# Kernel optimization log

Measured on AMD Instinct MI355X. Metric: run time of the kernel, lower is better.

Reference implementation:

```python
import jax, jax.numpy as jnp
import numpy as np

# Dimensions / config (WorldModelConfig + PredictiveLayerConfig defaults)
S, N, L = 128, 256, 3          # n_sensory, n_hidden, n_layers
T, B = 100, 512                # timesteps, batch
TAU_MEM, TAU_PRED, DT = 20.0, 50.0, 1.0
NOISE_STD, ERROR_GAIN = 0.02, 0.5
DECAY_MEM = float(np.exp(-DT / TAU_MEM))
DECAY_PRED = float(np.exp(-DT / TAU_PRED))
ALPHA = DT / TAU_PRED          # precision EMA rate


def setup_inputs() -> dict:
    key = jax.random.key(0)
    ks = jax.random.split(key, 12)
    w = lambda k, a, b, s: jax.random.normal(k, (a, b), dtype=jnp.float32) * s
    return {
        'sensory_seq': jax.random.uniform(ks[0], (T, B, S), dtype=jnp.float32),
        'ff0': w(ks[1], S, N, 0.1 / S ** 0.5),
        'ff1': w(ks[2], N, N, 0.1 / N ** 0.5),
        'ff2': w(ks[3], N, N, 0.1 / N ** 0.5),
        'rec0': w(ks[4], N, N, 0.01),
        'rec1': w(ks[5], N, N, 0.01),
        'rec2': w(ks[6], N, N, 0.01),
        'pred0': w(ks[7], N, N, 0.1 / N ** 0.5),
        'pred1': w(ks[8], N, N, 0.1 / N ** 0.5),
        'p2r0': w(ks[9], N, N, 0.1 / N ** 0.5),
        'p2r1': w(ks[10], N, N, 0.1 / N ** 0.5),
    }


def _lif(v, inp, decay, noise):
    """LIF membrane update: leak + drive + noise, threshold=1.0, reset to 0."""
    v = decay * v + inp + noise
    s = (v >= 1.0).astype(v.dtype)
    return s, v * (1.0 - s)


def reference(sensory_seq, ff0, ff1, ff2, rec0, rec1, rec2, pred0, pred1, p2r0, p2r1):
    ffs = [ff0, ff1, ff2]
    recs = [rec0, rec1, rec2]
    preds = [pred0, pred1]
    p2rs = [p2r0, p2r1]
    mask = 1.0 - jnp.eye(N, dtype=sensory_seq.dtype)   # recurrent_mask
    base_key = jax.random.key(42)
    Bsz = sensory_seq.shape[1]

    init = (
        jnp.zeros((L, Bsz, N), jnp.float32),   # repr membrane
        jnp.zeros((2, Bsz, N), jnp.float32),   # pred membrane (layers 0,1)
        jnp.zeros((L, Bsz, N), jnp.float32),   # last spikes
        jnp.ones((L, Bsz, N), jnp.float32),    # precision
    )

    def step(carry, t):
        v, pv, last, prec = carry
        nks = jax.random.split(jax.random.fold_in(base_key, t), 5)
        new_v, new_pv, new_last, new_prec, errs = [], [], [], [], []
        for i in range(L):
            # top-down prediction from layer i+1's previous-step activity
            if i < L - 1:
                pred_in = last[i + 1] @ preds[i]
                pn = (NOISE_STD * 0.5) * jax.random.normal(nks[3 + i], (Bsz, N))
                psp, pvi = _lif(pv[i], pred_in, DECAY_PRED, pn)
                prediction = psp @ p2rs[i]
                new_pv.append(pvi)
            else:
                prediction = jnp.zeros((Bsz, N), jnp.float32)
            # bottom-up input: sensory for layer 0, lower layer's current spikes above
            inp_act = sensory_seq[t] if i == 0 else new_last[i - 1]
            input_repr = inp_act @ ffs[i]
            error = input_repr - prediction
            total = prediction + error * ERROR_GAIN * prec[i] + last[i] @ (recs[i] * mask)
            noi = NOISE_STD * jax.random.normal(nks[i], (Bsz, N))
            sp, vi = _lif(v[i], total, DECAY_MEM, noi)
            # precision EMA on inverse error variance
            ev = jnp.mean(error * error, axis=1, keepdims=True) + 1e-6
            pr = (1.0 - ALPHA) * prec[i] + ALPHA * (1.0 / ev)
            new_v.append(vi); new_last.append(sp); new_prec.append(pr); errs.append(error)
        carry = (jnp.stack(new_v), jnp.stack(new_pv), jnp.stack(new_last), jnp.stack(new_prec))
        return carry, jnp.stack(errs)   # [L, B, N] per step

    _, errors = jax.lax.scan(step, init, jnp.arange(T))
    return errors   # [T, L, B, N]
```

## Files before the change

kernel.cpp:

```cpp
#include <hip/hip_runtime.h>
#include <stdint.h>

#define TSTEPS 100
#define BATCH  512
#define NH     256
#define NS     128

__device__ __forceinline__ uint32_t rotl32(uint32_t x, int r) {
  return (x << r) | (x >> (32 - r));
}

__device__ __forceinline__ void tf2x32(uint32_t k0, uint32_t k1,
                                       uint32_t c0, uint32_t c1,
                                       uint32_t& o0, uint32_t& o1) {
  const uint32_t ks2 = k0 ^ k1 ^ 0x1BD11BDAu;
  uint32_t x0 = c0 + k0, x1 = c1 + k1;
#define TFR(r) { x0 += x1; x1 = rotl32(x1, r); x1 ^= x0; }
  TFR(13) TFR(15) TFR(26) TFR(6)
  x0 += k1;  x1 += ks2 + 1u;
  TFR(17) TFR(29) TFR(16) TFR(24)
  x0 += ks2; x1 += k0 + 2u;
  TFR(13) TFR(15) TFR(26) TFR(6)
  x0 += k0;  x1 += k1 + 3u;
  TFR(17) TFR(29) TFR(16) TFR(24)
  x0 += k1;  x1 += ks2 + 4u;
  TFR(13) TFR(15) TFR(26) TFR(6)
  x0 += ks2; x1 += k0 + 5u;
#undef TFR
  o0 = x0; o1 = x1;
}

__device__ __forceinline__ float xla_vf32_log(float a) {
  uint32_t bits = __float_as_uint(a);
  float e = __fadd_rn((float)((int)(bits >> 23) - 127), 1.0f);
  float x = __uint_as_float((bits & 0x007FFFFFu) | 0x3F000000u);
  const bool mask = x < 0.707106781186547524f;
  float tmp = mask ? x : 0.0f;
  x = __fsub_rn(x, 1.0f);
  e = mask ? __fsub_rn(e, 1.0f) : e;
  x = __fadd_rn(x, tmp);
  float z = __fmul_rn(x, x);
  float y = 7.0376836292e-2f;
  y = __fmaf_rn(y, x, -1.1514610310e-1f);
  y = __fmaf_rn(y, x, 1.1676998740e-1f);
  y = __fmaf_rn(y, x, -1.2420140846e-1f);
  y = __fmaf_rn(y, x, 1.4249322787e-1f);
  y = __fmaf_rn(y, x, -1.6668057665e-1f);
  y = __fmaf_rn(y, x, 2.0000714765e-1f);
  y = __fmaf_rn(y, x, -2.4999993993e-1f);
  y = __fmaf_rn(y, x, 3.3333331174e-1f);
  y = __fmul_rn(y, x);
  y = __fmul_rn(y, z);
  y = __fmaf_rn(e, -2.12194440e-4f, y);
  y = __fmaf_rn(-0.5f, z, y);
  x = __fadd_rn(x, y);
  x = __fmaf_rn(e, 0.693359375f, x);
  return x;
}

__device__ __forceinline__ float xla_sqrt2_erfinv(float u) {
  float nxx = -__fmul_rn(u, u);
  float w;
  if (fabsf(nxx) < 1e-4f) {
    w = -__fmul_rn(__fmaf_rn(-0.5f, nxx, 1.0f), nxx);
  } else {
    w = -xla_vf32_log(__fadd_rn(nxx, 1.0f));
  }
  float p;
  if (w < 5.0f) {
    float t = __fsub_rn(w, 2.5f);
    p = 2.81022636e-08f;
    p = __fmaf_rn(p, t, 3.43273939e-07f);
    p = __fmaf_rn(p, t, -3.5233877e-06f);
    p = __fmaf_rn(p, t, -4.39150654e-06f);
    p = __fmaf_rn(p, t, 0.00021858087f);
    p = __fmaf_rn(p, t, -0.00125372503f);
    p = __fmaf_rn(p, t, -0.00417768164f);
    p = __fmaf_rn(p, t, 0.246640727f);
    p = __fmaf_rn(p, t, 1.50140941f);
  } else {
    float t = __fsub_rn(__fsqrt_rn(w), 3.0f);
    p = -0.000200214257f;
    p = __fmaf_rn(p, t, 0.000100950558f);
    p = __fmaf_rn(p, t, 0.00134934322f);
    p = __fmaf_rn(p, t, -0.00367342844f);
    p = __fmaf_rn(p, t, 0.00573950773f);
    p = __fmaf_rn(p, t, -0.0076224613f);
    p = __fmaf_rn(p, t, 0.00943887047f);
    p = __fmaf_rn(p, t, 1.00167406f);
    p = __fmaf_rn(p, t, 2.83297682f);
  }
  return __fmul_rn((float)1.4142135623730951, __fmul_rn(p, u));
}

__device__ __forceinline__ float jax_normal(uint32_t k0, uint32_t k1, uint32_t j) {
  uint32_t o0, o1;
  tf2x32(k0, k1, 0u, j, o0, o1);
  const uint32_t bits = o0 ^ o1;
  float f = __fsub_rn(__uint_as_float((bits >> 9) | 0x3f800000u), 1.0f);
  const float LO = -0.99999994f;
  float u = __fmaf_rn(f, 2.0f, LO);
  u = fmaxf(LO, u);
  return xla_sqrt2_erfinv(u);
}


__device__ __forceinline__ void dot1_seg(const float4* __restrict__ P0,
                                         const float* __restrict__ A0,
                                         int n, int k4b, int k4e, float& r0) {
  float a0 = r0;
  #pragma unroll 8
  for (int k4 = k4b; k4 < k4e; ++k4) {
    float4 w0 = P0[k4 * NH + n];
    float4 x0 = *reinterpret_cast<const float4*>(A0 + 4 * k4);
    a0 = __fmaf_rn(x0.x, w0.x, a0); a0 = __fmaf_rn(x0.y, w0.y, a0);
    a0 = __fmaf_rn(x0.z, w0.z, a0); a0 = __fmaf_rn(x0.w, w0.w, a0);
  }
  r0 = a0;
}

__device__ __forceinline__ void dot2_seg(const float4* __restrict__ P0,
                                         const float* __restrict__ A0,
                                         const float4* __restrict__ P1,
                                         const float* __restrict__ A1,
                                         int n, int k4b, int k4e,
                                         float& r0, float& r1) {
  float a0 = r0, a1 = r1;
  #pragma unroll 8
  for (int k4 = k4b; k4 < k4e; ++k4) {
    float4 w0 = P0[k4 * NH + n];
    float4 w1 = P1[k4 * NH + n];
    float4 x0 = *reinterpret_cast<const float4*>(A0 + 4 * k4);
    float4 x1 = *reinterpret_cast<const float4*>(A1 + 4 * k4);
    a0 = __fmaf_rn(x0.x, w0.x, a0); a0 = __fmaf_rn(x0.y, w0.y, a0);
    a0 = __fmaf_rn(x0.z, w0.z, a0); a0 = __fmaf_rn(x0.w, w0.w, a0);
    a1 = __fmaf_rn(x1.x, w1.x, a1); a1 = __fmaf_rn(x1.y, w1.y, a1);
    a1 = __fmaf_rn(x1.z, w1.z, a1); a1 = __fmaf_rn(x1.w, w1.w, a1);
  }
  r0 = a0; r1 = a1;
}

__device__ __forceinline__ void dot3_seg(const float4* __restrict__ P0,
                                         const float* __restrict__ A0,
                                         const float4* __restrict__ P1,
                                         const float* __restrict__ A1,
                                         const float4* __restrict__ P2,
                                         const float* __restrict__ A2,
                                         int n, int k4b, int k4e,
                                         float& r0, float& r1, float& r2) {
  float a0 = r0, a1 = r1, a2 = r2;
  #pragma unroll 4
  for (int k4 = k4b; k4 < k4e; ++k4) {
    float4 w0 = P0[k4 * NH + n];
    float4 w1 = P1[k4 * NH + n];
    float4 w2 = P2[k4 * NH + n];
    float4 x0 = *reinterpret_cast<const float4*>(A0 + 4 * k4);
    float4 x1 = *reinterpret_cast<const float4*>(A1 + 4 * k4);
    float4 x2 = *reinterpret_cast<const float4*>(A2 + 4 * k4);
    a0 = __fmaf_rn(x0.x, w0.x, a0); a0 = __fmaf_rn(x0.y, w0.y, a0);
    a0 = __fmaf_rn(x0.z, w0.z, a0); a0 = __fmaf_rn(x0.w, w0.w, a0);
    a1 = __fmaf_rn(x1.x, w1.x, a1); a1 = __fmaf_rn(x1.y, w1.y, a1);
    a1 = __fmaf_rn(x1.z, w1.z, a1); a1 = __fmaf_rn(x1.w, w1.w, a1);
    a2 = __fmaf_rn(x2.x, w2.x, a2); a2 = __fmaf_rn(x2.y, w2.y, a2);
    a2 = __fmaf_rn(x2.z, w2.z, a2); a2 = __fmaf_rn(x2.w, w2.w, a2);
  }
  r0 = a0; r1 = a1; r2 = a2;
}

__global__ void pack_w(const float* __restrict__ src, float* __restrict__ dst,
                       int K, int zero_diag) {
  int tid = blockIdx.x * 256 + threadIdx.x;
  if (tid >= K * NH) return;
  int k = tid >> 8, n = tid & 255;
  float v = src[tid];
  if (zero_diag && k == n) v = 0.f;
  dst[(((k >> 2) * NH) + n) * 4 + (k & 3)] = v;
}

__global__ __launch_bounds__(256)
void gen_noise(float* __restrict__ NZ) {
  uint32_t idx = blockIdx.x * 256u + threadIdx.x;
  uint32_t j = idx & 131071u;
  uint32_t td = idx >> 17;
  uint32_t t = td / 5u, d = td - 5u * t;
  uint32_t fk0, fk1, k0, k1;
  tf2x32(0u, 42u, 0u, t, fk0, fk1);
  tf2x32(fk0, fk1, 0u, d, k0, k1);
  float z = jax_normal(k0, k1, j);
  float scale = (d >= 3u) ? 0.01f : 0.02f;
  NZ[idx] = __fmul_rn(scale, z);
}

__global__ __launch_bounds__(NH)
void wm_kernel_fast(const float* __restrict__ sensory,
                    const float4* __restrict__ pred0p, const float4* __restrict__ pred1p,
                    const float4* __restrict__ p2r0p,  const float4* __restrict__ rec0p,
                    const float4* __restrict__ ff0p,   const float4* __restrict__ p2r1p,
                    const float4* __restrict__ ff1p,   const float4* __restrict__ rec1p,
                    const float4* __restrict__ ff2p,   const float4* __restrict__ rec2p,
                    const float* __restrict__ NZ,
                    float* __restrict__ out) {
  const int b = blockIdx.x;
  const int n = threadIdx.x;

  __shared__ __align__(16) float last[2][3][NH];
  __shared__ __align__(16) float psp0[NH];
  __shared__ __align__(16) float psp1[NH];
  __shared__ __align__(16) float sens[NS];
  __shared__ __align__(16) float errsq[3][NH];
  __shared__ float evsum[3];

  for (int i = 0; i < 3; ++i) { last[0][i][n] = 0.f; last[1][i][n] = 0.f; }

  float v0 = 0.f, v1 = 0.f, v2 = 0.f, pv0 = 0.f, pv1 = 0.f;
  float prec0 = 1.f, prec1 = 1.f, prec2 = 1.f;
  const float DM = (float)0.951229424500714009;
  const float DP = (float)0.980198673306755250;

  __syncthreads();

  for (int t = 0; t < TSTEPS; ++t) {
    const int p = t & 1, q = p ^ 1;
    const size_t nb = ((size_t)t * 5 * BATCH + b) * NH + n;

    if (n < NS) sens[n] = sensory[((size_t)t * BATCH + b) * NS + n];
    {
      float pn0 = NZ[nb + (size_t)3 * BATCH * NH];
      float pn1 = NZ[nb + (size_t)4 * BATCH * NH];
      float acc0 = 0.f, acc1 = 0.f;
      dot2_seg(pred0p, last[p][1], pred1p, last[p][2], n, 0, 64, acc0, acc1);
      pv0 = __fadd_rn(__fmaf_rn(DP, pv0, acc0), pn0);
      bool s0 = (pv0 >= 1.0f);
      psp0[n] = s0 ? 1.f : 0.f;
      pv0 = s0 ? 0.f : pv0;
      pv1 = __fadd_rn(__fmaf_rn(DP, pv1, acc1), pn1);
      bool s1 = (pv1 >= 1.0f);
      psp1[n] = s1 ? 1.f : 0.f;
      pv1 = s1 ? 0.f : pv1;
    }
    __syncthreads();

    {
      float noi = NZ[nb];
      float pr = 0.f, rc = 0.f, inp = 0.f;
      dot3_seg(p2r0p, psp0, rec0p, last[p][0], ff0p, sens, n, 0, 32, pr, rc, inp);
      dot2_seg(p2r0p, psp0, rec0p, last[p][0], n, 32, 64, pr, rc);
      float err = __fsub_rn(inp, pr);
      out[(((size_t)t * 3 + 0) * BATCH + b) * NH + n] = err;
      errsq[0][n] = __fmul_rn(err, err);
      float m1  = __fmul_rn(err, 0.5f);
      float tot = __fadd_rn(__fmaf_rn(m1, prec0, pr), rc);
      v0 = __fadd_rn(__fmaf_rn(DM, v0, tot), noi);
      bool s = (v0 >= 1.0f);
      last[q][0][n] = s ? 1.f : 0.f;
      v0 = s ? 0.f : v0;
    }
    __syncthreads();

    {
      float noi = NZ[nb + (size_t)1 * BATCH * NH];
      float pr = 0.f, inp = 0.f, rc = 0.f;
      dot3_seg(p2r1p, psp1, ff1p, last[q][0], rec1p, last[p][1], n, 0, 64,
               pr, inp, rc);
      float err = __fsub_rn(inp, pr);
      out[(((size_t)t * 3 + 1) * BATCH + b) * NH + n] = err;
      errsq[1][n] = __fmul_rn(err, err);
      float m1  = __fmul_rn(err, 0.5f);
      float tot = __fadd_rn(__fmaf_rn(m1, prec1, pr), rc);
      v1 = __fadd_rn(__fmaf_rn(DM, v1, tot), noi);
      bool s = (v1 >= 1.0f);
      last[q][1][n] = s ? 1.f : 0.f;
      v1 = s ? 0.f : v1;
    }
    __syncthreads();

    {
      float noi = NZ[nb + (size_t)2 * BATCH * NH];
      float inp = 0.f, rc = 0.f;
      dot2_seg(ff2p, last[q][1], rec2p, last[p][2], n, 0, 64, inp, rc);
      float err = inp;
      out[(((size_t)t * 3 + 2) * BATCH + b) * NH + n] = err;
      errsq[2][n] = __fmul_rn(err, err);
      float m1  = __fmul_rn(err, 0.5f);
      float tot = __fadd_rn(__fmaf_rn(m1, prec2, 0.0f), rc);
      v2 = __fadd_rn(__fmaf_rn(DM, v2, tot), noi);
      bool s = (v2 >= 1.0f);
      last[q][2][n] = s ? 1.f : 0.f;
      v2 = s ? 0.f : v2;
    }
    __syncthreads();

    if (((n & 63) == 0) && n < 192) {
      const float4* s4 = reinterpret_cast<const float4*>(errsq[n >> 6]);
      float acc = 0.f;
      #pragma unroll 16
      for (int k4 = 0; k4 < 64; ++k4) {
        float4 v = s4[k4];
        acc = __fadd_rn(acc, v.x); acc = __fadd_rn(acc, v.y);
        acc = __fadd_rn(acc, v.z); acc = __fadd_rn(acc, v.w);
      }
      evsum[n >> 6] = acc;
    }
    __syncthreads();

    {
      float ev0 = __fadd_rn(__fmul_rn(evsum[0], 0.00390625f), 1e-6f);
      float ev1 = __fadd_rn(__fmul_rn(evsum[1], 0.00390625f), 1e-6f);
      float ev2 = __fadd_rn(__fmul_rn(evsum[2], 0.00390625f), 1e-6f);
      prec0 = __fmaf_rn(0.98f, prec0, __fmul_rn(0.02f, 1.0f / ev0));
      prec1 = __fmaf_rn(0.98f, prec1, __fmul_rn(0.02f, 1.0f / ev1));
      prec2 = __fmaf_rn(0.98f, prec2, __fmul_rn(0.02f, 1.0f / ev2));
    }
  }
}

__device__ __forceinline__ float dot_lds(const float* __restrict__ a,
                                         const float* __restrict__ W,
                                         int n, int K) {
  float acc = 0.f;
  #pragma unroll 8
  for (int k = 0; k < K; ++k)
    acc = __fmaf_rn(a[k], W[k * NH + n], acc);
  return acc;
}

__device__ __forceinline__ float dot_rec(const float* __restrict__ a,
                                         const float* __restrict__ W, int n) {
  float acc = 0.f;
  #pragma unroll 8
  for (int k = 0; k < NH; ++k) {
    float w = (k == n) ? 0.f : W[k * NH + n];
    acc = __fmaf_rn(a[k], w, acc);
  }
  return acc;
}

__global__ __launch_bounds__(NH)
void wm_kernel_mono(const float* __restrict__ sensory,
                    const float* __restrict__ ff0, const float* __restrict__ ff1,
                    const float* __restrict__ ff2,
                    const float* __restrict__ rec0, const float* __restrict__ rec1,
                    const float* __restrict__ rec2,
                    const float* __restrict__ pred0, const float* __restrict__ pred1,
                    const float* __restrict__ p2r0, const float* __restrict__ p2r1,
                    float* __restrict__ out) {
  const int b = blockIdx.x;
  const int n = threadIdx.x;

  __shared__ float last[2][3][NH];
  __shared__ float psp[NH];
  __shared__ float sens[NS];
  __shared__ float errsq[3][NH];
  __shared__ float evsum[3];
  __shared__ uint32_t keys[TSTEPS][5][2];

  if (n < TSTEPS) {
    uint32_t fk0, fk1;
    tf2x32(0u, 42u, 0u, (uint32_t)n, fk0, fk1);
    #pragma unroll
    for (int i = 0; i < 5; ++i) {
      uint32_t s0, s1;
      tf2x32(fk0, fk1, 0u, (uint32_t)i, s0, s1);
      keys[n][i][0] = s0; keys[n][i][1] = s1;
    }
  }
  for (int i = 0; i < 3; ++i) { last[0][i][n] = 0.f; last[1][i][n] = 0.f; }

  float v0 = 0.f, v1 = 0.f, v2 = 0.f, pv0 = 0.f, pv1 = 0.f;
  float prec0 = 1.f, prec1 = 1.f, prec2 = 1.f;
  const float DM = (float)0.951229424500714009;
  const float DP = (float)0.980198673306755250;
  const uint32_t j = (uint32_t)(b * NH + n);

  __syncthreads();

  for (int t = 0; t < TSTEPS; ++t) {
    const int p = t & 1, q = p ^ 1;

    if (n < NS) sens[n] = sensory[((size_t)t * BATCH + b) * NS + n];
    {
      float acc = dot_lds(last[p][1], pred0, n, NH);
      float pn = __fmul_rn(0.01f, jax_normal(keys[t][3][0], keys[t][3][1], j));
      pv0 = __fadd_rn(__fmaf_rn(DP, pv0, acc), pn);
      bool s = (pv0 >= 1.0f);
      psp[n] = s ? 1.f : 0.f;
      pv0 = s ? 0.f : pv0;
    }
    __syncthreads();

    {
      float pr  = dot_lds(psp, p2r0, n, NH);
      float inp = dot_lds(sens, ff0, n, NS);
      float rc  = dot_rec(last[p][0], rec0, n);
      float err = __fsub_rn(inp, pr);
      out[(((size_t)t * 3 + 0) * BATCH + b) * NH + n] = err;
      errsq[0][n] = __fmul_rn(err, err);
      float m1  = __fmul_rn(err, 0.5f);
      float tot = __fadd_rn(__fmaf_rn(m1, prec0, pr), rc);
      float noi = __fmul_rn(0.02f, jax_normal(keys[t][0][0], keys[t][0][1], j));
      v0 = __fadd_rn(__fmaf_rn(DM, v0, tot), noi);
      bool s = (v0 >= 1.0f);
      last[q][0][n] = s ? 1.f : 0.f;
      v0 = s ? 0.f : v0;
    }
    __syncthreads();

    {
      float acc = dot_lds(last[p][2], pred1, n, NH);
      float pn = __fmul_rn(0.01f, jax_normal(keys[t][4][0], keys[t][4][1], j));
      pv1 = __fadd_rn(__fmaf_rn(DP, pv1, acc), pn);
      bool s = (pv1 >= 1.0f);
      psp[n] = s ? 1.f : 0.f;
      pv1 = s ? 0.f : pv1;
    }
    __syncthreads();

    {
      float pr  = dot_lds(psp, p2r1, n, NH);
      float inp = dot_lds(last[q][0], ff1, n, NH);
      float rc  = dot_rec(last[p][1], rec1, n);
      float err = __fsub_rn(inp, pr);
      out[(((size_t)t * 3 + 1) * BATCH + b) * NH + n] = err;
      errsq[1][n] = __fmul_rn(err, err);
      float m1  = __fmul_rn(err, 0.5f);
      float tot = __fadd_rn(__fmaf_rn(m1, prec1, pr), rc);
      float noi = __fmul_rn(0.02f, jax_normal(keys[t][1][0], keys[t][1][1], j));
      v1 = __fadd_rn(__fmaf_rn(DM, v1, tot), noi);
      bool s = (v1 >= 1.0f);
      last[q][1][n] = s ? 1.f : 0.f;
      v1 = s ? 0.f : v1;
    }
    __syncthreads();

    {
      float inp = dot_lds(last[q][1], ff2, n, NH);
      float rc  = dot_rec(last[p][2], rec2, n);
      float err = inp;
      out[(((size_t)t * 3 + 2) * BATCH + b) * NH + n] = err;
      errsq[2][n] = __fmul_rn(err, err);
      float m1  = __fmul_rn(err, 0.5f);
      float tot = __fadd_rn(__fmaf_rn(m1, prec2, 0.0f), rc);
      float noi = __fmul_rn(0.02f, jax_normal(keys[t][2][0], keys[t][2][1], j));
      v2 = __fadd_rn(__fmaf_rn(DM, v2, tot), noi);
      bool s = (v2 >= 1.0f);
      last[q][2][n] = s ? 1.f : 0.f;
      v2 = s ? 0.f : v2;
    }
    __syncthreads();

    if (((n & 63) == 0) && n < 192) {
      const float* s = errsq[n >> 6];
      float acc = 0.f;
      #pragma unroll 32
      for (int k = 0; k < NH; ++k) acc = __fadd_rn(acc, s[k]);
      evsum[n >> 6] = acc;
    }
    __syncthreads();

    {
      float ev0 = __fadd_rn(__fmul_rn(evsum[0], 0.00390625f), 1e-6f);
      float ev1 = __fadd_rn(__fmul_rn(evsum[1], 0.00390625f), 1e-6f);
      float ev2 = __fadd_rn(__fmul_rn(evsum[2], 0.00390625f), 1e-6f);
      prec0 = __fmaf_rn(0.98f, prec0, __fmul_rn(0.02f, 1.0f / ev0));
      prec1 = __fmaf_rn(0.98f, prec1, __fmul_rn(0.02f, 1.0f / ev1));
      prec2 = __fmaf_rn(0.98f, prec2, __fmul_rn(0.02f, 1.0f / ev2));
    }
  }
}

extern "C" void kernel_launch(void* const* d_in, const int* in_sizes, int n_in,
                              void* d_out, int out_size, void* d_ws, size_t ws_size,
                              hipStream_t stream) {
  (void)in_sizes; (void)n_in; (void)out_size;
  const float* sensory = (const float*)d_in[0];
  const float* ff0  = (const float*)d_in[1];
  const float* ff1  = (const float*)d_in[2];
  const float* ff2  = (const float*)d_in[3];
  const float* rec0 = (const float*)d_in[4];
  const float* rec1 = (const float*)d_in[5];
  const float* rec2 = (const float*)d_in[6];
  const float* pred0 = (const float*)d_in[7];
  const float* pred1 = (const float*)d_in[8];
  const float* p2r0 = (const float*)d_in[9];
  const float* p2r1 = (const float*)d_in[10];
  float* out = (float*)d_out;

  const size_t OFF_PRED0 = 0, OFF_PRED1 = 65536, OFF_P2R0 = 131072,
               OFF_REC0 = 196608, OFF_FF0 = 262144, OFF_P2R1 = 294912,
               OFF_FF1 = 360448, OFF_REC1 = 425984, OFF_FF2 = 491520,
               OFF_REC2 = 557056, OFF_NZ = 655360;
  const size_t NZ_FLOATS = (size_t)TSTEPS * 5 * BATCH * NH;
  const size_t NEED = (OFF_NZ + NZ_FLOATS) * sizeof(float);

  if (ws_size >= NEED) {
    float* W = (float*)d_ws;
    pack_w<<<dim3(NH * NH / 256), dim3(256), 0, stream>>>(pred0, W + OFF_PRED0, NH, 0);
    pack_w<<<dim3(NH * NH / 256), dim3(256), 0, stream>>>(pred1, W + OFF_PRED1, NH, 0);
    pack_w<<<dim3(NH * NH / 256), dim3(256), 0, stream>>>(p2r0,  W + OFF_P2R0,  NH, 0);
    pack_w<<<dim3(NH * NH / 256), dim3(256), 0, stream>>>(rec0,  W + OFF_REC0,  NH, 1);
    pack_w<<<dim3(NS * NH / 256), dim3(256), 0, stream>>>(ff0,   W + OFF_FF0,   NS, 0);
    pack_w<<<dim3(NH * NH / 256), dim3(256), 0, stream>>>(p2r1,  W + OFF_P2R1,  NH, 0);
    pack_w<<<dim3(NH * NH / 256), dim3(256), 0, stream>>>(ff1,   W + OFF_FF1,   NH, 0);
    pack_w<<<dim3(NH * NH / 256), dim3(256), 0, stream>>>(rec1,  W + OFF_REC1,  NH, 1);
    pack_w<<<dim3(NH * NH / 256), dim3(256), 0, stream>>>(ff2,   W + OFF_FF2,   NH, 0);
    pack_w<<<dim3(NH * NH / 256), dim3(256), 0, stream>>>(rec2,  W + OFF_REC2,  NH, 1);
    gen_noise<<<dim3((unsigned)(NZ_FLOATS / 256)), dim3(256), 0, stream>>>(W + OFF_NZ);
    wm_kernel_fast<<<dim3(BATCH), dim3(NH), 0, stream>>>(
        sensory,
        (const float4*)(W + OFF_PRED0), (const float4*)(W + OFF_PRED1),
        (const float4*)(W + OFF_P2R0),  (const float4*)(W + OFF_REC0),
        (const float4*)(W + OFF_FF0),   (const float4*)(W + OFF_P2R1),
        (const float4*)(W + OFF_FF1),   (const float4*)(W + OFF_REC1),
        (const float4*)(W + OFF_FF2),   (const float4*)(W + OFF_REC2),
        W + OFF_NZ, out);
  } else {
    wm_kernel_mono<<<dim3(BATCH), dim3(NH), 0, stream>>>(
        sensory, ff0, ff1, ff2, rec0, rec1, rec2,
        pred0, pred1, p2r0, p2r1, out);
  }
}
```

Before: 4.600 ms.

## Process two batch rows per block so paired lanes share weight loads

Replaces the one-batch-per-block kernel with a 512-thread block handling two batch rows, interleaving lanes so neighbouring threads compute the same hidden unit for different rows. Weight float4 loads are shared across the lane pair, aiming to halve weight fetch traffic per output. In exchange, output and noise accesses become interleaved across rows (less contiguous), and block-level syncs now cover twice the threads.

```diff
diff --git a/kernel.cpp b/kernel.cpp
--- a/kernel.cpp
+++ b/kernel.cpp
@@ -104,6 +104,29 @@
   return xla_sqrt2_erfinv(u);
 }
 
+__global__ void pack_w(const float* __restrict__ src, float* __restrict__ dst,
+                       int K, int zero_diag) {
+  int tid = blockIdx.x * 256 + threadIdx.x;
+  if (tid >= K * NH) return;
+  int k = tid >> 8, n = tid & 255;
+  float v = src[tid];
+  if (zero_diag && k == n) v = 0.f;
+  dst[(((k >> 2) * NH) + n) * 4 + (k & 3)] = v;
+}
+
+__global__ __launch_bounds__(256)
+void gen_noise(float* __restrict__ NZ) {
+  uint32_t idx = blockIdx.x * 256u + threadIdx.x;
+  uint32_t j = idx & 131071u;
+  uint32_t td = idx >> 17;
+  uint32_t t = td / 5u, d = td - 5u * t;
+  uint32_t fk0, fk1, k0, k1;
+  tf2x32(0u, 42u, 0u, t, fk0, fk1);
+  tf2x32(fk0, fk1, 0u, d, k0, k1);
+  float z = jax_normal(k0, k1, j);
+  float scale = (d >= 3u) ? 0.01f : 0.02f;
+  NZ[idx] = __fmul_rn(scale, z);
+}
 
 __device__ __forceinline__ void dot1_seg(const float4* __restrict__ P0,
                                          const float* __restrict__ A0,
@@ -167,50 +190,32 @@
   r0 = a0; r1 = a1; r2 = a2;
 }
 
-__global__ void pack_w(const float* __restrict__ src, float* __restrict__ dst,
-                       int K, int zero_diag) {
-  int tid = blockIdx.x * 256 + threadIdx.x;
-  if (tid >= K * NH) return;
-  int k = tid >> 8, n = tid & 255;
-  float v = src[tid];
-  if (zero_diag && k == n) v = 0.f;
-  dst[(((k >> 2) * NH) + n) * 4 + (k & 3)] = v;
-}
-
-__global__ __launch_bounds__(256)
-void gen_noise(float* __restrict__ NZ) {
-  uint32_t idx = blockIdx.x * 256u + threadIdx.x;
-  uint32_t j = idx & 131071u;
-  uint32_t td = idx >> 17;
-  uint32_t t = td / 5u, d = td - 5u * t;
-  uint32_t fk0, fk1, k0, k1;
-  tf2x32(0u, 42u, 0u, t, fk0, fk1);
-  tf2x32(fk0, fk1, 0u, d, k0, k1);
-  float z = jax_normal(k0, k1, j);
-  float scale = (d >= 3u) ? 0.01f : 0.02f;
-  NZ[idx] = __fmul_rn(scale, z);
-}
-
-__global__ __launch_bounds__(NH)
-void wm_kernel_fast(const float* __restrict__ sensory,
-                    const float4* __restrict__ pred0p, const float4* __restrict__ pred1p,
-                    const float4* __restrict__ p2r0p,  const float4* __restrict__ rec0p,
-                    const float4* __restrict__ ff0p,   const float4* __restrict__ p2r1p,
-                    const float4* __restrict__ ff1p,   const float4* __restrict__ rec1p,
-                    const float4* __restrict__ ff2p,   const float4* __restrict__ rec2p,
-                    const float* __restrict__ NZ,
-                    float* __restrict__ out) {
-  const int b = blockIdx.x;
-  const int n = threadIdx.x;
-
-  __shared__ __align__(16) float last[2][3][NH];
-  __shared__ __align__(16) float psp0[NH];
-  __shared__ __align__(16) float psp1[NH];
-  __shared__ __align__(16) float sens[NS];
-  __shared__ __align__(16) float errsq[3][NH];
-  __shared__ float evsum[3];
-
-  for (int i = 0; i < 3; ++i) { last[0][i][n] = 0.f; last[1][i][n] = 0.f; }
+__global__ __launch_bounds__(512)
+void wm_fast4(const float* __restrict__ sensory,
+              const float4* __restrict__ pred0p, const float4* __restrict__ pred1p,
+              const float4* __restrict__ p2r0p,  const float4* __restrict__ rec0p,
+              const float4* __restrict__ ff0p,   const float4* __restrict__ p2r1p,
+              const float4* __restrict__ ff1p,   const float4* __restrict__ rec1p,
+              const float4* __restrict__ ff2p,   const float4* __restrict__ rec2p,
+              const float* __restrict__ NZ,
+              float* __restrict__ out) {
+  const int tid = threadIdx.x;
+  const int n = tid >> 1;
+  const int r = tid & 1;
+  const int b = blockIdx.x * 2 + r;
+
+  __shared__ __align__(16) float last[2][3][2][NH];
+  __shared__ __align__(16) float psp0[2][NH];
+  __shared__ __align__(16) float psp1[2][NH];
+  __shared__ __align__(16) float sens[2][NS];
+  __shared__ __align__(16) float errsq[3][2][NH];
+  __shared__ float evsum[3][2];
+
+  #pragma unroll
+  for (int i = 0; i < 3; ++i) {
+    last[0][i][r][n] = 0.f;
+    last[1][i][r][n] = 0.f;
+  }
 
   float v0 = 0.f, v1 = 0.f, v2 = 0.f, pv0 = 0.f, pv1 = 0.f;
   float prec0 = 1.f, prec1 = 1.f, prec2 = 1.f;
@@ -223,19 +228,22 @@
     const int p = t & 1, q = p ^ 1;
     const size_t nb = ((size_t)t * 5 * BATCH + b) * NH + n;
 
-    if (n < NS) sens[n] = sensory[((size_t)t * BATCH + b) * NS + n];
+    if (tid < 2 * NS) {
+      int rr = tid >> 7, kk = tid & 127;
+      sens[rr][kk] = sensory[((size_t)t * BATCH + blockIdx.x * 2 + rr) * NS + kk];
+    }
     {
       float pn0 = NZ[nb + (size_t)3 * BATCH * NH];
       float pn1 = NZ[nb + (size_t)4 * BATCH * NH];
       float acc0 = 0.f, acc1 = 0.f;
-      dot2_seg(pred0p, last[p][1], pred1p, last[p][2], n, 0, 64, acc0, acc1);
+      dot2_seg(pred0p, last[p][1][r], pred1p, last[p][2][r], n, 0, 64, acc0, acc1);
       pv0 = __fadd_rn(__fmaf_rn(DP, pv0, acc0), pn0);
       bool s0 = (pv0 >= 1.0f);
-      psp0[n] = s0 ? 1.f : 0.f;
+      psp0[r][n] = s0 ? 1.f : 0.f;
       pv0 = s0 ? 0.f : pv0;
       pv1 = __fadd_rn(__fmaf_rn(DP, pv1, acc1), pn1);
       bool s1 = (pv1 >= 1.0f);
-      psp1[n] = s1 ? 1.f : 0.f;
+      psp1[r][n] = s1 ? 1.f : 0.f;
       pv1 = s1 ? 0.f : pv1;
     }
     __syncthreads();
@@ -243,16 +251,17 @@
     {
       float noi = NZ[nb];
       float pr = 0.f, rc = 0.f, inp = 0.f;
-      dot3_seg(p2r0p, psp0, rec0p, last[p][0], ff0p, sens, n, 0, 32, pr, rc, inp);
-      dot2_seg(p2r0p, psp0, rec0p, last[p][0], n, 32, 64, pr, rc);
+      dot3_seg(p2r0p, psp0[r], rec0p, last[p][0][r], ff0p, sens[r], n, 0, 32,
+               pr, rc, inp);
+      dot2_seg(p2r0p, psp0[r], rec0p, last[p][0][r], n, 32, 64, pr, rc);
       float err = __fsub_rn(inp, pr);
       out[(((size_t)t * 3 + 0) * BATCH + b) * NH + n] = err;
-      errsq[0][n] = __fmul_rn(err, err);
+      errsq[0][r][n] = __fmul_rn(err, err);
       float m1  = __fmul_rn(err, 0.5f);
       float tot = __fadd_rn(__fmaf_rn(m1, prec0, pr), rc);
       v0 = __fadd_rn(__fmaf_rn(DM, v0, tot), noi);
       bool s = (v0 >= 1.0f);
-      last[q][0][n] = s ? 1.f : 0.f;
+      last[q][0][r][n] = s ? 1.f : 0.f;
       v0 = s ? 0.f : v0;
     }
     __syncthreads();
@@ -260,16 +269,16 @@
     {
       float noi = NZ[nb + (size_t)1 * BATCH * NH];
       float pr = 0.f, inp = 0.f, rc = 0.f;
-      dot3_seg(p2r1p, psp1, ff1p, last[q][0], rec1p, last[p][1], n, 0, 64,
-               pr, inp, rc);
+      dot3_seg(p2r1p, psp1[r], ff1p, last[q][0][r], rec1p, last[p][1][r],
+               n, 0, 64, pr, inp, rc);
       float err = __fsub_rn(inp, pr);
       out[(((size_t)t * 3 + 1) * BATCH + b) * NH + n] = err;
-      errsq[1][n] = __fmul_rn(err, err);
+      errsq[1][r][n] = __fmul_rn(err, err);
       float m1  = __fmul_rn(err, 0.5f);
       float tot = __fadd_rn(__fmaf_rn(m1, prec1, pr), rc);
       v1 = __fadd_rn(__fmaf_rn(DM, v1, tot), noi);
       bool s = (v1 >= 1.0f);
-      last[q][1][n] = s ? 1.f : 0.f;
+      last[q][1][r][n] = s ? 1.f : 0.f;
       v1 = s ? 0.f : v1;
     }
     __syncthreads();
@@ -277,21 +286,22 @@
     {
       float noi = NZ[nb + (size_t)2 * BATCH * NH];
       float inp = 0.f, rc = 0.f;
-      dot2_seg(ff2p, last[q][1], rec2p, last[p][2], n, 0, 64, inp, rc);
+      dot2_seg(ff2p, last[q][1][r], rec2p, last[p][2][r], n, 0, 64, inp, rc);
       float err = inp;
       out[(((size_t)t * 3 + 2) * BATCH + b) * NH + n] = err;
-      errsq[2][n] = __fmul_rn(err, err);
+      errsq[2][r][n] = __fmul_rn(err, err);
       float m1  = __fmul_rn(err, 0.5f);
       float tot = __fadd_rn(__fmaf_rn(m1, prec2, 0.0f), rc);
       v2 = __fadd_rn(__fmaf_rn(DM, v2, tot), noi);
       bool s = (v2 >= 1.0f);
-      last[q][2][n] = s ? 1.f : 0.f;
+      last[q][2][r][n] = s ? 1.f : 0.f;
       v2 = s ? 0.f : v2;
     }
     __syncthreads();
 
-    if (((n & 63) == 0) && n < 192) {
-      const float4* s4 = reinterpret_cast<const float4*>(errsq[n >> 6]);
+    if (tid < 6) {
+      const int l = tid >> 1, rr = tid & 1;
+      const float4* s4 = reinterpret_cast<const float4*>(errsq[l][rr]);
       float acc = 0.f;
       #pragma unroll 16
       for (int k4 = 0; k4 < 64; ++k4) {
@@ -299,14 +309,14 @@
         acc = __fadd_rn(acc, v.x); acc = __fadd_rn(acc, v.y);
         acc = __fadd_rn(acc, v.z); acc = __fadd_rn(acc, v.w);
       }
-      evsum[n >> 6] = acc;
-    }
-    __syncthreads();
-
-    {
-      float ev0 = __fadd_rn(__fmul_rn(evsum[0], 0.00390625f), 1e-6f);
-      float ev1 = __fadd_rn(__fmul_rn(evsum[1], 0.00390625f), 1e-6f);
-      float ev2 = __fadd_rn(__fmul_rn(evsum[2], 0.00390625f), 1e-6f);
+      evsum[l][rr] = acc;
+    }
+    __syncthreads();
+
+    {
+      float ev0 = __fadd_rn(__fmul_rn(evsum[0][r], 0.00390625f), 1e-6f);
+      float ev1 = __fadd_rn(__fmul_rn(evsum[1][r], 0.00390625f), 1e-6f);
+      float ev2 = __fadd_rn(__fmul_rn(evsum[2][r], 0.00390625f), 1e-6f);
       prec0 = __fmaf_rn(0.98f, prec0, __fmul_rn(0.02f, 1.0f / ev0));
       prec1 = __fmaf_rn(0.98f, prec1, __fmul_rn(0.02f, 1.0f / ev1));
       prec2 = __fmaf_rn(0.98f, prec2, __fmul_rn(0.02f, 1.0f / ev2));
@@ -505,7 +515,7 @@
     pack_w<<<dim3(NH * NH / 256), dim3(256), 0, stream>>>(ff2,   W + OFF_FF2,   NH, 0);
     pack_w<<<dim3(NH * NH / 256), dim3(256), 0, stream>>>(rec2,  W + OFF_REC2,  NH, 1);
     gen_noise<<<dim3((unsigned)(NZ_FLOATS / 256)), dim3(256), 0, stream>>>(W + OFF_NZ);
-    wm_kernel_fast<<<dim3(BATCH), dim3(NH), 0, stream>>>(
+    wm_fast4<<<dim3(BATCH / 2), dim3(512), 0, stream>>>(
         sensory,
         (const float4*)(W + OFF_PRED0), (const float4*)(W + OFF_PRED1),
         (const float4*)(W + OFF_P2R0),  (const float4*)(W + OFF_REC0),
```

Result: no change. 4.554 ms (-1.0%).

## Split each batch row's matvecs across two 256-thread halves per block

Applied to the files above, without the earlier changes.

Doubles the block size to 512 threads, so two half-blocks each handle one output neuron and share the per-step matrix-vector products. Partial results are exchanged through a shared-memory transfer buffer. This shortens the serial dot-product chain each thread runs per timestep and raises the number of waves per CU. The cost is extra barriers per step, idle halves during the elementwise updates, and more register and occupancy pressure with 512-thread blocks.

```diff
diff --git a/kernel.cpp b/kernel.cpp
--- a/kernel.cpp
+++ b/kernel.cpp
@@ -104,6 +104,29 @@
   return xla_sqrt2_erfinv(u);
 }
 
+__global__ void pack_w(const float* __restrict__ src, float* __restrict__ dst,
+                       int K, int zero_diag) {
+  int tid = blockIdx.x * 256 + threadIdx.x;
+  if (tid >= K * NH) return;
+  int k = tid >> 8, n = tid & 255;
+  float v = src[tid];
+  if (zero_diag && k == n) v = 0.f;
+  dst[(((k >> 2) * NH) + n) * 4 + (k & 3)] = v;
+}
+
+__global__ __launch_bounds__(256)
+void gen_noise(float* __restrict__ NZ) {
+  uint32_t idx = blockIdx.x * 256u + threadIdx.x;
+  uint32_t j = idx & 131071u;
+  uint32_t td = idx >> 17;
+  uint32_t t = td / 5u, d = td - 5u * t;
+  uint32_t fk0, fk1, k0, k1;
+  tf2x32(0u, 42u, 0u, t, fk0, fk1);
+  tf2x32(fk0, fk1, 0u, d, k0, k1);
+  float z = jax_normal(k0, k1, j);
+  float scale = (d >= 3u) ? 0.01f : 0.02f;
+  NZ[idx] = __fmul_rn(scale, z);
+}
 
 __device__ __forceinline__ void dot1_seg(const float4* __restrict__ P0,
                                          const float* __restrict__ A0,
@@ -140,79 +163,34 @@
   r0 = a0; r1 = a1;
 }
 
-__device__ __forceinline__ void dot3_seg(const float4* __restrict__ P0,
-                                         const float* __restrict__ A0,
-                                         const float4* __restrict__ P1,
-                                         const float* __restrict__ A1,
-                                         const float4* __restrict__ P2,
-                                         const float* __restrict__ A2,
-                                         int n, int k4b, int k4e,
-                                         float& r0, float& r1, float& r2) {
-  float a0 = r0, a1 = r1, a2 = r2;
-  #pragma unroll 4
-  for (int k4 = k4b; k4 < k4e; ++k4) {
-    float4 w0 = P0[k4 * NH + n];
-    float4 w1 = P1[k4 * NH + n];
-    float4 w2 = P2[k4 * NH + n];
-    float4 x0 = *reinterpret_cast<const float4*>(A0 + 4 * k4);
-    float4 x1 = *reinterpret_cast<const float4*>(A1 + 4 * k4);
-    float4 x2 = *reinterpret_cast<const float4*>(A2 + 4 * k4);
-    a0 = __fmaf_rn(x0.x, w0.x, a0); a0 = __fmaf_rn(x0.y, w0.y, a0);
-    a0 = __fmaf_rn(x0.z, w0.z, a0); a0 = __fmaf_rn(x0.w, w0.w, a0);
-    a1 = __fmaf_rn(x1.x, w1.x, a1); a1 = __fmaf_rn(x1.y, w1.y, a1);
-    a1 = __fmaf_rn(x1.z, w1.z, a1); a1 = __fmaf_rn(x1.w, w1.w, a1);
-    a2 = __fmaf_rn(x2.x, w2.x, a2); a2 = __fmaf_rn(x2.y, w2.y, a2);
-    a2 = __fmaf_rn(x2.z, w2.z, a2); a2 = __fmaf_rn(x2.w, w2.w, a2);
-  }
-  r0 = a0; r1 = a1; r2 = a2;
-}
-
-__global__ void pack_w(const float* __restrict__ src, float* __restrict__ dst,
-                       int K, int zero_diag) {
-  int tid = blockIdx.x * 256 + threadIdx.x;
-  if (tid >= K * NH) return;
-  int k = tid >> 8, n = tid & 255;
-  float v = src[tid];
-  if (zero_diag && k == n) v = 0.f;
-  dst[(((k >> 2) * NH) + n) * 4 + (k & 3)] = v;
-}
-
-__global__ __launch_bounds__(256)
-void gen_noise(float* __restrict__ NZ) {
-  uint32_t idx = blockIdx.x * 256u + threadIdx.x;
-  uint32_t j = idx & 131071u;
-  uint32_t td = idx >> 17;
-  uint32_t t = td / 5u, d = td - 5u * t;
-  uint32_t fk0, fk1, k0, k1;
-  tf2x32(0u, 42u, 0u, t, fk0, fk1);
-  tf2x32(fk0, fk1, 0u, d, k0, k1);
-  float z = jax_normal(k0, k1, j);
-  float scale = (d >= 3u) ? 0.01f : 0.02f;
-  NZ[idx] = __fmul_rn(scale, z);
-}
-
-__global__ __launch_bounds__(NH)
-void wm_kernel_fast(const float* __restrict__ sensory,
-                    const float4* __restrict__ pred0p, const float4* __restrict__ pred1p,
-                    const float4* __restrict__ p2r0p,  const float4* __restrict__ rec0p,
-                    const float4* __restrict__ ff0p,   const float4* __restrict__ p2r1p,
-                    const float4* __restrict__ ff1p,   const float4* __restrict__ rec1p,
-                    const float4* __restrict__ ff2p,   const float4* __restrict__ rec2p,
-                    const float* __restrict__ NZ,
-                    float* __restrict__ out) {
+__global__ __launch_bounds__(512)
+void wm_fast5(const float* __restrict__ sensory,
+              const float4* __restrict__ pred0p, const float4* __restrict__ pred1p,
+              const float4* __restrict__ p2r0p,  const float4* __restrict__ rec0p,
+              const float4* __restrict__ ff0p,   const float4* __restrict__ p2r1p,
+              const float4* __restrict__ ff1p,   const float4* __restrict__ rec1p,
+              const float4* __restrict__ ff2p,   const float4* __restrict__ rec2p,
+              const float* __restrict__ NZ,
+              float* __restrict__ out) {
+  const int tid = threadIdx.x;
+  const int n = tid & 255;
+  const int h = tid >> 8;
   const int b = blockIdx.x;
-  const int n = threadIdx.x;
 
   __shared__ __align__(16) float last[2][3][NH];
   __shared__ __align__(16) float psp0[NH];
   __shared__ __align__(16) float psp1[NH];
   __shared__ __align__(16) float sens[NS];
   __shared__ __align__(16) float errsq[3][NH];
+  __shared__ __align__(16) float xfer[NH];
   __shared__ float evsum[3];
 
-  for (int i = 0; i < 3; ++i) { last[0][i][n] = 0.f; last[1][i][n] = 0.f; }
-
-  float v0 = 0.f, v1 = 0.f, v2 = 0.f, pv0 = 0.f, pv1 = 0.f;
+  if (h == 0) {
+    #pragma unroll
+    for (int i = 0; i < 3; ++i) { last[0][i][n] = 0.f; last[1][i][n] = 0.f; }
+  }
+
+  float pv = 0.f, vA = 0.f, vB = 0.f;
   float prec0 = 1.f, prec1 = 1.f, prec2 = 1.f;
   const float DM = (float)0.951229424500714009;
   const float DP = (float)0.980198673306755250;
@@ -223,75 +201,104 @@
     const int p = t & 1, q = p ^ 1;
     const size_t nb = ((size_t)t * 5 * BATCH + b) * NH + n;
 
-    if (n < NS) sens[n] = sensory[((size_t)t * BATCH + b) * NS + n];
-    {
-      float pn0 = NZ[nb + (size_t)3 * BATCH * NH];
-      float pn1 = NZ[nb + (size_t)4 * BATCH * NH];
-      float acc0 = 0.f, acc1 = 0.f;
-      dot2_seg(pred0p, last[p][1], pred1p, last[p][2], n, 0, 64, acc0, acc1);
-      pv0 = __fadd_rn(__fmaf_rn(DP, pv0, acc0), pn0);
-      bool s0 = (pv0 >= 1.0f);
-      psp0[n] = s0 ? 1.f : 0.f;
-      pv0 = s0 ? 0.f : pv0;
-      pv1 = __fadd_rn(__fmaf_rn(DP, pv1, acc1), pn1);
-      bool s1 = (pv1 >= 1.0f);
-      psp1[n] = s1 ? 1.f : 0.f;
-      pv1 = s1 ? 0.f : pv1;
-    }
-    __syncthreads();
-
-    {
+    if (tid < NS) sens[tid] = sensory[((size_t)t * BATCH + b) * NS + tid];
+    if (h == 0) {
+      float acc = 0.f;
+      dot1_seg(pred0p, last[p][1], n, 0, 64, acc);
+      float pn = NZ[nb + (size_t)3 * BATCH * NH];
+      pv = __fadd_rn(__fmaf_rn(DP, pv, acc), pn);
+      bool s = (pv >= 1.0f);
+      psp0[n] = s ? 1.f : 0.f;
+      pv = s ? 0.f : pv;
+    } else {
+      float acc = 0.f;
+      dot1_seg(pred1p, last[p][2], n, 0, 64, acc);
+      float pn = NZ[nb + (size_t)4 * BATCH * NH];
+      pv = __fadd_rn(__fmaf_rn(DP, pv, acc), pn);
+      bool s = (pv >= 1.0f);
+      psp1[n] = s ? 1.f : 0.f;
+      pv = s ? 0.f : pv;
+    }
+    __syncthreads();
+
+    float inp_b = 0.f, rc_b = 0.f;
+    if (h == 0) {
+      dot2_seg(ff0p, sens, rec0p, last[p][0], n, 0, 32, inp_b, rc_b);
+      dot1_seg(rec0p, last[p][0], n, 32, 64, rc_b);
+    } else {
+      float pr = 0.f;
+      dot1_seg(p2r0p, psp0, n, 0, 64, pr);
+      xfer[n] = pr;
+    }
+    __syncthreads();
+    if (h == 0) {
+      float pr = xfer[n];
       float noi = NZ[nb];
-      float pr = 0.f, rc = 0.f, inp = 0.f;
-      dot3_seg(p2r0p, psp0, rec0p, last[p][0], ff0p, sens, n, 0, 32, pr, rc, inp);
-      dot2_seg(p2r0p, psp0, rec0p, last[p][0], n, 32, 64, pr, rc);
-      float err = __fsub_rn(inp, pr);
+      float err = __fsub_rn(inp_b, pr);
       out[(((size_t)t * 3 + 0) * BATCH + b) * NH + n] = err;
       errsq[0][n] = __fmul_rn(err, err);
       float m1  = __fmul_rn(err, 0.5f);
-      float tot = __fadd_rn(__fmaf_rn(m1, prec0, pr), rc);
-      v0 = __fadd_rn(__fmaf_rn(DM, v0, tot), noi);
-      bool s = (v0 >= 1.0f);
+      float tot = __fadd_rn(__fmaf_rn(m1, prec0, pr), rc_b);
+      vA = __fadd_rn(__fmaf_rn(DM, vA, tot), noi);
+      bool s = (vA >= 1.0f);
       last[q][0][n] = s ? 1.f : 0.f;
-      v0 = s ? 0.f : v0;
-    }
-    __syncthreads();
-
-    {
+      vA = s ? 0.f : vA;
+    }
+    __syncthreads();
+
+    if (h == 0) {
+      float inp = 0.f;
+      dot1_seg(ff1p, last[q][0], n, 0, 64, inp);
+      xfer[n] = inp;
+    } else {
+      float pr = 0.f, rc = 0.f;
+      dot2_seg(p2r1p, psp1, rec1p, last[p][1], n, 0, 64, pr, rc);
+      inp_b = pr; rc_b = rc;
+    }
+    __syncthreads();
+    if (h == 1) {
+      float pr = inp_b, rc = rc_b;
+      float inp = xfer[n];
       float noi = NZ[nb + (size_t)1 * BATCH * NH];
-      float pr = 0.f, inp = 0.f, rc = 0.f;
-      dot3_seg(p2r1p, psp1, ff1p, last[q][0], rec1p, last[p][1], n, 0, 64,
-               pr, inp, rc);
       float err = __fsub_rn(inp, pr);
       out[(((size_t)t * 3 + 1) * BATCH + b) * NH + n] = err;
       errsq[1][n] = __fmul_rn(err, err);
       float m1  = __fmul_rn(err, 0.5f);
       float tot = __fadd_rn(__fmaf_rn(m1, prec1, pr), rc);
-      v1 = __fadd_rn(__fmaf_rn(DM, v1, tot), noi);
-      bool s = (v1 >= 1.0f);
+      vA = __fadd_rn(__fmaf_rn(DM, vA, tot), noi);
+      bool s = (vA >= 1.0f);
       last[q][1][n] = s ? 1.f : 0.f;
-      v1 = s ? 0.f : v1;
-    }
-    __syncthreads();
-
-    {
+      vA = s ? 0.f : vA;
+    }
+    __syncthreads();
+
+    if (h == 0) {
+      float inp = 0.f;
+      dot1_seg(ff2p, last[q][1], n, 0, 64, inp);
+      inp_b = inp;
+    } else {
+      float rc = 0.f;
+      dot1_seg(rec2p, last[p][2], n, 0, 64, rc);
+      xfer[n] = rc;
+    }
+    __syncthreads();
+    if (h == 0) {
+      float rc = xfer[n];
+      float err = inp_b;
       float noi = NZ[nb + (size_t)2 * BATCH * NH];
-      float inp = 0.f, rc = 0.f;
-      dot2_seg(ff2p, last[q][1], rec2p, last[p][2], n, 0, 64, inp, rc);
-      float err = inp;
       out[(((size_t)t * 3 + 2) * BATCH + b) * NH + n] = err;
       errsq[2][n] = __fmul_rn(err, err);
       float m1  = __fmul_rn(err, 0.5f);
       float tot = __fadd_rn(__fmaf_rn(m1, prec2, 0.0f), rc);
-      v2 = __fadd_rn(__fmaf_rn(DM, v2, tot), noi);
-      bool s = (v2 >= 1.0f);
+      vB = __fadd_rn(__fmaf_rn(DM, vB, tot), noi);
+      bool s = (vB >= 1.0f);
       last[q][2][n] = s ? 1.f : 0.f;
-      v2 = s ? 0.f : v2;
-    }
-    __syncthreads();
-
-    if (((n & 63) == 0) && n < 192) {
-      const float4* s4 = reinterpret_cast<const float4*>(errsq[n >> 6]);
+      vB = s ? 0.f : vB;
+    }
+    __syncthreads();
+
+    if (((tid & 63) == 0) && tid < 192) {
+      const float4* s4 = reinterpret_cast<const float4*>(errsq[tid >> 6]);
       float acc = 0.f;
       #pragma unroll 16
       for (int k4 = 0; k4 < 64; ++k4) {
@@ -299,7 +306,7 @@
         acc = __fadd_rn(acc, v.x); acc = __fadd_rn(acc, v.y);
         acc = __fadd_rn(acc, v.z); acc = __fadd_rn(acc, v.w);
       }
-      evsum[n >> 6] = acc;
+      evsum[tid >> 6] = acc;
     }
     __syncthreads();
 
@@ -505,7 +512,7 @@
     pack_w<<<dim3(NH * NH / 256), dim3(256), 0, stream>>>(ff2,   W + OFF_FF2,   NH, 0);
     pack_w<<<dim3(NH * NH / 256), dim3(256), 0, stream>>>(rec2,  W + OFF_REC2,  NH, 1);
     gen_noise<<<dim3((unsigned)(NZ_FLOATS / 256)), dim3(256), 0, stream>>>(W + OFF_NZ);
-    wm_kernel_fast<<<dim3(BATCH), dim3(NH), 0, stream>>>(
+    wm_fast5<<<dim3(BATCH), dim3(512), 0, stream>>>(
         sensory,
         (const float4*)(W + OFF_PRED0), (const float4*)(W + OFF_PRED1),
         (const float4*)(W + OFF_P2R0),  (const float4*)(W + OFF_REC0),
```

New measurement: 4.691 ms. No clear change (+2.0%).
